# Performance work log

Measured on AMD Instinct MI355X. Metric: run time of the kernel, lower is better.

The kernel has to match this reference:

```python
import jax, jax.numpy as jnp
import numpy as np

N, D, T, E = 50000, 128, 6, 600000
LN_EPS = 1e-5


def setup_inputs() -> dict:
    key = jax.random.key(0)
    ks = jax.random.split(key, 8)
    x = jax.random.normal(ks[0], (N, D), dtype=jnp.float32)
    edge_index = jax.random.randint(ks[1], (2, E), 0, N, dtype=jnp.int64)
    edge_type = jax.random.randint(ks[2], (E,), 0, T, dtype=jnp.int64)
    s = 1.0 / np.sqrt(D)
    W_l = jax.random.normal(ks[3], (T, D, D), dtype=jnp.float32) * s
    W_r = jax.random.normal(ks[4], (T, D, D), dtype=jnp.float32) * s
    b = jax.random.normal(ks[5], (T, D), dtype=jnp.float32) * s
    emb = jax.random.normal(ks[6], (T, D), dtype=jnp.float32)
    gamma = jnp.ones((D,), dtype=jnp.float32)
    beta = jnp.zeros((D,), dtype=jnp.float32)
    return {"x": x, "edge_index": edge_index, "edge_type": edge_type,
            "W_l": W_l, "W_r": W_r, "b": b, "emb": emb,
            "gamma": gamma, "beta": beta}


def reference(x, edge_index, edge_type, W_l, W_r, b, emb, gamma, beta):
    n, d = x.shape
    t = W_l.shape[0]
    src, dst = edge_index[0], edge_index[1]
    # Combined segment id (dst, edge_type) -> one segment_sum for all types.
    seg = dst * t + edge_type
    msgs = x[src]  # (E, d) gathered source features
    sums = jax.ops.segment_sum(msgs, seg, num_segments=n * t).reshape(n, t, d)
    cnt = jax.ops.segment_sum(jnp.ones((seg.shape[0],), x.dtype), seg,
                              num_segments=n * t).reshape(n, t, 1)
    mean = sums / jnp.maximum(cnt, 1.0)  # PyG mean aggr: 0 for isolated nodes
    # Per-type SAGEConv: mean_t @ W_l[t] + x @ W_r[t] + b[t] + emb[t], summed over t.
    h = (jnp.einsum('ntd,tdo->no', mean, W_l)
         + x @ W_r.sum(0)
         + (b.sum(0) + emb.sum(0)))
    mu = jnp.mean(h, axis=-1, keepdims=True)
    var = jnp.var(h, axis=-1, keepdims=True)
    y = (h - mu) * jax.lax.rsqrt(var + LN_EPS) * gamma + beta
    return jax.nn.relu(y)
```

## Files before the change

kernel.cpp:

```cpp
#include <hip/hip_runtime.h>

#define TT 6
#define D 128
#define BM 64
#define CAP 1152
#define SUBCAP 256
#define LN_EPS 1e-5f

typedef __bf16 bf16x8 __attribute__((ext_vector_type(8)));
typedef float f32x4 __attribute__((ext_vector_type(4)));

__device__ __forceinline__ unsigned short f2bf(float f) {
    unsigned int u = __float_as_uint(f);
    unsigned int r = (u + 0x7FFFu + ((u >> 16) & 1u)) >> 16;
    return (unsigned short)r;
}
__device__ __forceinline__ float bflo(unsigned int v) { return __uint_as_float(v << 16); }
__device__ __forceinline__ float bfhi(unsigned int v) { return __uint_as_float(v & 0xffff0000u); }

__device__ __forceinline__ int lds_off128(int row, int kgrp) {
    return row * 128 + (((kgrp & 7) ^ (row & 7)) | (kgrp & 8)) * 8;
}

__global__ void prep_kernel(const float* __restrict__ x, const float* __restrict__ W_l,
                            const float* __restrict__ W_r, const float* __restrict__ b,
                            const float* __restrict__ emb,
                            const int* __restrict__ ei, const int* __restrict__ et,
                            unsigned short* __restrict__ xb, unsigned short* __restrict__ WlT,
                            float* __restrict__ bias_total, int* __restrict__ bcursor,
                            int* __restrict__ ebuf,
                            int total8, int E, int N, int NBK) {
    int i = blockIdx.x * 256 + threadIdx.x;
    if (i < total8) {
        const float4* p = (const float4*)x + (size_t)i * 2;
        float4 a = p[0], bb = p[1];
        uint4 o;
        o.x = (unsigned int)f2bf(a.x) | ((unsigned int)f2bf(a.y) << 16);
        o.y = (unsigned int)f2bf(a.z) | ((unsigned int)f2bf(a.w) << 16);
        o.z = (unsigned int)f2bf(bb.x) | ((unsigned int)f2bf(bb.y) << 16);
        o.w = (unsigned int)f2bf(bb.z) | ((unsigned int)f2bf(bb.w) << 16);
        ((uint4*)xb)[i] = o;
        return;
    }
    i -= total8;
    if (i < 7 * 2048) {
        int s = i >> 11, rem = i & 2047, kg = rem >> 7, n = rem & 127;
        float w[8];
        if (s < TT) {
#pragma unroll
            for (int j = 0; j < 8; ++j)
                w[j] = W_l[s * D * D + (kg * 8 + j) * D + n];
        } else {
#pragma unroll
            for (int j = 0; j < 8; ++j) {
                float sum = 0.f;
#pragma unroll
                for (int t = 0; t < TT; ++t)
                    sum += W_r[t * D * D + (kg * 8 + j) * D + n];
                w[j] = sum;
            }
        }
        uint4 o;
        o.x = (unsigned int)f2bf(w[0]) | ((unsigned int)f2bf(w[1]) << 16);
        o.y = (unsigned int)f2bf(w[2]) | ((unsigned int)f2bf(w[3]) << 16);
        o.z = (unsigned int)f2bf(w[4]) | ((unsigned int)f2bf(w[5]) << 16);
        o.w = (unsigned int)f2bf(w[6]) | ((unsigned int)f2bf(w[7]) << 16);
        *(uint4*)&WlT[(size_t)i * 8] = o;
        return;
    }
    i -= 7 * 2048;
    if (i < D) {
        float s = 0.f;
#pragma unroll
        for (int t = 0; t < TT; ++t) s += b[t * D + i] + emb[t * D + i];
        bias_total[i] = s;
        return;
    }
    i -= D;
    if (i < E) {
        int src = ei[i], dst = ei[E + i], t = et[i];
        int bkt = dst >> 6;
        int shard = blockIdx.x & 7;
        int pos = atomicAdd(&bcursor[(shard * NBK + bkt) * 16], 1);
        if (pos < SUBCAP)
            ebuf[(size_t)bkt * (8 * SUBCAP) + shard * SUBCAP + pos] =
                (src << 9) | ((dst & 63) << 3) | t;
    }
}

__launch_bounds__(256, 3)
__global__ void fused_kernel(const unsigned short* __restrict__ xb,
                             const int* __restrict__ bcursor, const int* __restrict__ ebuf,
                             const unsigned short* __restrict__ WlT,
                             const float* __restrict__ bias_total,
                             const float* __restrict__ gamma, const float* __restrict__ beta,
                             float* __restrict__ out, int N) {
    __shared__ unsigned short As[BM * 128];
    __shared__ int bcnt[TT * BM];
    __shared__ int bcur[TT * BM];
    __shared__ unsigned short esrt[CAP];

    int tid = threadIdx.x;
    int lane = tid & 63, wave = tid >> 6;
    int q = lane >> 4, c16 = lane & 15;
    int qid = tid >> 4, l16 = tid & 15;
    int blockRow = blockIdx.x * BM;
    int NBK = gridDim.x;

    size_t base = (size_t)blockIdx.x * (8 * SUBCAP);
#pragma unroll
    for (int j = 0; j < 2; ++j) {
        int idx = tid + j * 256;
        if (idx < TT * BM) { bcnt[idx] = 0; }
    }
    int pk[8];
#pragma unroll
    for (int j = 0; j < 8; ++j) {
        int bcj = bcursor[(j * NBK + blockIdx.x) * 16];
        if (bcj > SUBCAP) bcj = SUBCAP;
        pk[j] = (tid < bcj) ? ebuf[base + j * SUBCAP + tid] : -1;
    }
    __syncthreads();
#pragma unroll
    for (int j = 0; j < 8; ++j)
        if (pk[j] >= 0) atomicAdd(&bcnt[(pk[j] & 7) * 64 + ((pk[j] >> 3) & 63)], 1);
    __syncthreads();

    if (wave == 0) {
        int c[6];
        int ts = 0;
#pragma unroll
        for (int j = 0; j < 6; ++j) { c[j] = bcnt[lane * 6 + j]; ts += c[j]; }
        int inc = ts;
#pragma unroll
        for (int o = 1; o < 64; o <<= 1) {
            int n = __shfl_up(inc, o);
            if (lane >= o) inc += n;
        }
        int run = inc - ts;
#pragma unroll
        for (int j = 0; j < 6; ++j) { bcur[lane * 6 + j] = run; run += c[j]; }
    }
    __syncthreads();

#pragma unroll
    for (int j = 0; j < 8; ++j)
        if (pk[j] >= 0) {
            int s = (pk[j] & 7) * 64 + ((pk[j] >> 3) & 63);
            int p = atomicAdd(&bcur[s], 1);
            if (p < CAP) esrt[p] = (unsigned short)(pk[j] >> 9);
        }
    __syncthreads();

    f32x4 acc[8];
#pragma unroll
    for (int ct = 0; ct < 8; ++ct) acc[ct] = (f32x4){0.f, 0.f, 0.f, 0.f};

    const unsigned short* Bbase = WlT + ((size_t)q * 128 + c16) * 8;

#pragma unroll 1
    for (int t = 0; t < 7; ++t) {
        bf16x8 afx[4];
        if (t < TT) {
#pragma unroll
            for (int pr = 0; pr < 2; ++pr) {
                int e0[2], cn[2];
#pragma unroll
                for (int i = 0; i < 2; ++i) {
                    int row = qid * 4 + pr * 2 + i;
                    int s = t * 64 + row;
                    int c = bcnt[s];
                    cn[i] = c;
                    e0[i] = bcur[s] - c;
                }
                int ix[2][4];
#pragma unroll
                for (int i = 0; i < 2; ++i)
#pragma unroll
                    for (int j = 0; j < 4; ++j)
                        ix[i][j] = (cn[i] > j) ? (int)esrt[e0[i] + j] : 0;
                uint4 v[2][4];
#pragma unroll
                for (int i = 0; i < 2; ++i)
#pragma unroll
                    for (int j = 0; j < 4; ++j) {
                        v[i][j] = (uint4){0u, 0u, 0u, 0u};
                        if (cn[i] > j)
                            v[i][j] = *(const uint4*)(xb + (size_t)ix[i][j] * D + l16 * 8);
                    }
#pragma unroll
                for (int i = 0; i < 2; ++i) {
                    float a0 = bflo(v[i][0].x) + bflo(v[i][1].x) + bflo(v[i][2].x) + bflo(v[i][3].x);
                    float a1 = bfhi(v[i][0].x) + bfhi(v[i][1].x) + bfhi(v[i][2].x) + bfhi(v[i][3].x);
                    float a2 = bflo(v[i][0].y) + bflo(v[i][1].y) + bflo(v[i][2].y) + bflo(v[i][3].y);
                    float a3 = bfhi(v[i][0].y) + bfhi(v[i][1].y) + bfhi(v[i][2].y) + bfhi(v[i][3].y);
                    float a4 = bflo(v[i][0].z) + bflo(v[i][1].z) + bflo(v[i][2].z) + bflo(v[i][3].z);
                    float a5 = bfhi(v[i][0].z) + bfhi(v[i][1].z) + bfhi(v[i][2].z) + bfhi(v[i][3].z);
                    float a6 = bflo(v[i][0].w) + bflo(v[i][1].w) + bflo(v[i][2].w) + bflo(v[i][3].w);
                    float a7 = bfhi(v[i][0].w) + bfhi(v[i][1].w) + bfhi(v[i][2].w) + bfhi(v[i][3].w);
                    int e = e0[i] + 4, end = e0[i] + cn[i];
#pragma unroll 1
                    while (e < end) {
                        int s = (int)esrt[e++];
                        uint4 vv = *(const uint4*)(xb + (size_t)s * D + l16 * 8);
                        a0 += bflo(vv.x); a1 += bfhi(vv.x);
                        a2 += bflo(vv.y); a3 += bfhi(vv.y);
                        a4 += bflo(vv.z); a5 += bfhi(vv.z);
                        a6 += bflo(vv.w); a7 += bfhi(vv.w);
                    }
                    if (cn[i] > 1) {
                        float sc = 1.f / (float)cn[i];
                        a0 *= sc; a1 *= sc; a2 *= sc; a3 *= sc;
                        a4 *= sc; a5 *= sc; a6 *= sc; a7 *= sc;
                    }
                    uint4 p;
                    p.x = (unsigned int)f2bf(a0) | ((unsigned int)f2bf(a1) << 16);
                    p.y = (unsigned int)f2bf(a2) | ((unsigned int)f2bf(a3) << 16);
                    p.z = (unsigned int)f2bf(a4) | ((unsigned int)f2bf(a5) << 16);
                    p.w = (unsigned int)f2bf(a6) | ((unsigned int)f2bf(a7) << 16);
                    *(uint4*)&As[lds_off128(qid * 4 + pr * 2 + i, l16)] = p;
                }
            }
        } else {
            int gr = blockRow + wave * 16 + c16; if (gr >= N) gr = N - 1;
#pragma unroll
            for (int ks = 0; ks < 4; ++ks)
                afx[ks] = *(const bf16x8*)(xb + (size_t)gr * D + (ks * 4 + q) * 8);
        }

        const unsigned short* Bt = Bbase + (size_t)t * 16384;
#pragma unroll
        for (int ks = 0; ks < 4; ++ks) {
            bf16x8 af;
            if (t < TT)
                af = *(const bf16x8*)&As[lds_off128(wave * 16 + c16, ks * 4 + q)];
            else
                af = afx[ks];
#pragma unroll
            for (int ct = 0; ct < 8; ++ct) {
                bf16x8 bfr = *(const bf16x8*)(Bt + ks * 4096 + ct * 128);
                acc[ct] = __builtin_amdgcn_mfma_f32_16x16x32_bf16(af, bfr, acc[ct], 0, 0, 0);
            }
        }
    }

    float bias_c[8], g_c[8], bt_c[8];
#pragma unroll
    for (int ct = 0; ct < 8; ++ct) {
        int col = ct * 16 + c16;
        bias_c[ct] = bias_total[col];
        g_c[ct] = gamma[col];
        bt_c[ct] = beta[col];
    }
#pragma unroll
    for (int reg = 0; reg < 4; ++reg) {
        float h[8];
        float s = 0.f, s2 = 0.f;
#pragma unroll
        for (int ct = 0; ct < 8; ++ct) {
            h[ct] = acc[ct][reg] + bias_c[ct];
            s += h[ct];
            s2 += h[ct] * h[ct];
        }
#pragma unroll
        for (int o = 8; o >= 1; o >>= 1) {
            s  += __shfl_xor(s, o, 16);
            s2 += __shfl_xor(s2, o, 16);
        }
        float mu = s * (1.f / 128.f);
        float var = s2 * (1.f / 128.f) - mu * mu;
        float rstd = rsqrtf(var + LN_EPS);
        int row = blockRow + wave * 16 + q * 4 + reg;
        if (row < N) {
#pragma unroll
            for (int ct = 0; ct < 8; ++ct) {
                float y = (h[ct] - mu) * rstd * g_c[ct] + bt_c[ct];
                out[(size_t)row * D + ct * 16 + c16] = fmaxf(y, 0.f);
            }
        }
    }
}

extern "C" void kernel_launch(void* const* d_in, const int* in_sizes, int n_in,
                              void* d_out, int out_size, void* d_ws, size_t ws_size,
                              hipStream_t stream) {
    const float* x     = (const float*)d_in[0];
    const int*   ei    = (const int*)d_in[1];
    const int*   et    = (const int*)d_in[2];
    const float* W_l   = (const float*)d_in[3];
    const float* W_r   = (const float*)d_in[4];
    const float* b     = (const float*)d_in[5];
    const float* emb   = (const float*)d_in[6];
    const float* gamma = (const float*)d_in[7];
    const float* beta  = (const float*)d_in[8];

    int N = in_sizes[0] / D;
    int E = in_sizes[2];
    int NBLK = (N + BM - 1) / BM;

    int* bcursor = (int*)d_ws;
    int* ebuf    = bcursor + 8 * NBLK * 16;
    size_t ofs = (size_t)((char*)(ebuf + (size_t)NBLK * 8 * SUBCAP) - (char*)d_ws);
    ofs = (ofs + 15) & ~(size_t)15;
    unsigned short* WlT = (unsigned short*)((char*)d_ws + ofs);
    float* bias_total = (float*)(WlT + 7 * 2048 * 8);
    size_t ofs2 = (size_t)((char*)(bias_total + D) - (char*)d_ws);
    ofs2 = (ofs2 + 15) & ~(size_t)15;
    unsigned short* xb = (unsigned short*)((char*)d_ws + ofs2);

    hipMemsetAsync(bcursor, 0, (size_t)(8 * NBLK * 16) * sizeof(int), stream);

    int total8 = N * D / 8;
    int G = total8 + 7 * 2048 + D + E;
    prep_kernel<<<(G + 255) / 256, 256, 0, stream>>>(x, W_l, W_r, b, emb, ei, et,
                                                     xb, WlT, bias_total, bcursor, ebuf,
                                                     total8, E, N, NBLK);

    fused_kernel<<<NBLK, 256, 0, stream>>>(xb, bcursor, ebuf, WlT, bias_total,
                                           gamma, beta, (float*)d_out, N);
}
```

Before: 182.2 us.

## Merge prep and fused kernels into one persistent kernel with grid barrier

Folds the preprocessing work (bf16 conversion of x and weights, bias sum, edge bucketing) into the main kernel as a grid-stride loop. A software global barrier on an atomic counter separates it from the aggregation/GEMM/LayerNorm phase. This removes one kernel launch and the gap between launches. The barrier relies on all 782 blocks being co-resident; at 3 blocks/CU on 256 CUs that holds, but otherwise it would deadlock. The shard index now depends on a different block mapping, which changes sub-bucket contention.

```diff
diff --git a/kernel.cpp b/kernel.cpp
--- a/kernel.cpp
+++ b/kernel.cpp
@@ -22,92 +22,96 @@
     return row * 128 + (((kgrp & 7) ^ (row & 7)) | (kgrp & 8)) * 8;
 }
 
-__global__ void prep_kernel(const float* __restrict__ x, const float* __restrict__ W_l,
+__launch_bounds__(256, 3)
+__global__ void mega_kernel(const float* __restrict__ x, const float* __restrict__ W_l,
                             const float* __restrict__ W_r, const float* __restrict__ b,
                             const float* __restrict__ emb,
                             const int* __restrict__ ei, const int* __restrict__ et,
                             unsigned short* __restrict__ xb, unsigned short* __restrict__ WlT,
                             float* __restrict__ bias_total, int* __restrict__ bcursor,
-                            int* __restrict__ ebuf,
-                            int total8, int E, int N, int NBK) {
-    int i = blockIdx.x * 256 + threadIdx.x;
-    if (i < total8) {
-        const float4* p = (const float4*)x + (size_t)i * 2;
-        float4 a = p[0], bb = p[1];
-        uint4 o;
-        o.x = (unsigned int)f2bf(a.x) | ((unsigned int)f2bf(a.y) << 16);
-        o.y = (unsigned int)f2bf(a.z) | ((unsigned int)f2bf(a.w) << 16);
-        o.z = (unsigned int)f2bf(bb.x) | ((unsigned int)f2bf(bb.y) << 16);
-        o.w = (unsigned int)f2bf(bb.z) | ((unsigned int)f2bf(bb.w) << 16);
-        ((uint4*)xb)[i] = o;
-        return;
-    }
-    i -= total8;
-    if (i < 7 * 2048) {
-        int s = i >> 11, rem = i & 2047, kg = rem >> 7, n = rem & 127;
-        float w[8];
-        if (s < TT) {
-#pragma unroll
-            for (int j = 0; j < 8; ++j)
-                w[j] = W_l[s * D * D + (kg * 8 + j) * D + n];
-        } else {
-#pragma unroll
-            for (int j = 0; j < 8; ++j) {
-                float sum = 0.f;
-#pragma unroll
-                for (int t = 0; t < TT; ++t)
-                    sum += W_r[t * D * D + (kg * 8 + j) * D + n];
-                w[j] = sum;
-            }
-        }
-        uint4 o;
-        o.x = (unsigned int)f2bf(w[0]) | ((unsigned int)f2bf(w[1]) << 16);
-        o.y = (unsigned int)f2bf(w[2]) | ((unsigned int)f2bf(w[3]) << 16);
-        o.z = (unsigned int)f2bf(w[4]) | ((unsigned int)f2bf(w[5]) << 16);
-        o.w = (unsigned int)f2bf(w[6]) | ((unsigned int)f2bf(w[7]) << 16);
-        *(uint4*)&WlT[(size_t)i * 8] = o;
-        return;
-    }
-    i -= 7 * 2048;
-    if (i < D) {
-        float s = 0.f;
-#pragma unroll
-        for (int t = 0; t < TT; ++t) s += b[t * D + i] + emb[t * D + i];
-        bias_total[i] = s;
-        return;
-    }
-    i -= D;
-    if (i < E) {
-        int src = ei[i], dst = ei[E + i], t = et[i];
-        int bkt = dst >> 6;
-        int shard = blockIdx.x & 7;
-        int pos = atomicAdd(&bcursor[(shard * NBK + bkt) * 16], 1);
-        if (pos < SUBCAP)
-            ebuf[(size_t)bkt * (8 * SUBCAP) + shard * SUBCAP + pos] =
-                (src << 9) | ((dst & 63) << 3) | t;
-    }
-}
-
-__launch_bounds__(256, 3)
-__global__ void fused_kernel(const unsigned short* __restrict__ xb,
-                             const int* __restrict__ bcursor, const int* __restrict__ ebuf,
-                             const unsigned short* __restrict__ WlT,
-                             const float* __restrict__ bias_total,
-                             const float* __restrict__ gamma, const float* __restrict__ beta,
-                             float* __restrict__ out, int N) {
+                            int* __restrict__ gctr, int* __restrict__ ebuf,
+                            const float* __restrict__ gamma, const float* __restrict__ beta,
+                            float* __restrict__ out,
+                            int total8, int E, int N) {
     __shared__ unsigned short As[BM * 128];
     __shared__ int bcnt[TT * BM];
     __shared__ int bcur[TT * BM];
     __shared__ unsigned short esrt[CAP];
 
     int tid = threadIdx.x;
+    int bid = blockIdx.x;
+    int NBK = gridDim.x;
+
+    int G = total8 + 7 * 2048 + D + E;
+    int stride = NBK * 256;
+    for (int i = bid * 256 + tid; i < G; i += stride) {
+        int j = i;
+        if (j < total8) {
+            const float4* p = (const float4*)x + (size_t)j * 2;
+            float4 a = p[0], bb = p[1];
+            uint4 o;
+            o.x = (unsigned int)f2bf(a.x) | ((unsigned int)f2bf(a.y) << 16);
+            o.y = (unsigned int)f2bf(a.z) | ((unsigned int)f2bf(a.w) << 16);
+            o.z = (unsigned int)f2bf(bb.x) | ((unsigned int)f2bf(bb.y) << 16);
+            o.w = (unsigned int)f2bf(bb.z) | ((unsigned int)f2bf(bb.w) << 16);
+            ((uint4*)xb)[j] = o;
+        } else if ((j -= total8) < 7 * 2048) {
+            int s = j >> 11, rem = j & 2047, kg = rem >> 7, n = rem & 127;
+            float w[8];
+            if (s < TT) {
+#pragma unroll
+                for (int k = 0; k < 8; ++k)
+                    w[k] = W_l[s * D * D + (kg * 8 + k) * D + n];
+            } else {
+#pragma unroll
+                for (int k = 0; k < 8; ++k) {
+                    float sum = 0.f;
+#pragma unroll
+                    for (int t = 0; t < TT; ++t)
+                        sum += W_r[t * D * D + (kg * 8 + k) * D + n];
+                    w[k] = sum;
+                }
+            }
+            uint4 o;
+            o.x = (unsigned int)f2bf(w[0]) | ((unsigned int)f2bf(w[1]) << 16);
+            o.y = (unsigned int)f2bf(w[2]) | ((unsigned int)f2bf(w[3]) << 16);
+            o.z = (unsigned int)f2bf(w[4]) | ((unsigned int)f2bf(w[5]) << 16);
+            o.w = (unsigned int)f2bf(w[6]) | ((unsigned int)f2bf(w[7]) << 16);
+            *(uint4*)&WlT[(size_t)j * 8] = o;
+        } else if ((j -= 7 * 2048) < D) {
+            float s = 0.f;
+#pragma unroll
+            for (int t = 0; t < TT; ++t) s += b[t * D + j] + emb[t * D + j];
+            bias_total[j] = s;
+        } else {
+            j -= D;
+            int src = ei[j], dst = ei[E + j], t = et[j];
+            int bkt = dst >> 6;
+            int shard = bid & 7;
+            int pos = atomicAdd(&bcursor[(shard * NBK + bkt) * 16], 1);
+            if (pos < SUBCAP)
+                ebuf[(size_t)bkt * (8 * SUBCAP) + shard * SUBCAP + pos] =
+                    (src << 9) | ((dst & 63) << 3) | t;
+        }
+    }
+
+    __syncthreads();
+    if (tid == 0) {
+        __threadfence();
+        atomicAdd(gctr, 1);
+        while (atomicAdd(gctr, 0) < (int)gridDim.x) {
+            __builtin_amdgcn_s_sleep(2);
+        }
+        __threadfence();
+    }
+    __syncthreads();
+
     int lane = tid & 63, wave = tid >> 6;
     int q = lane >> 4, c16 = lane & 15;
     int qid = tid >> 4, l16 = tid & 15;
-    int blockRow = blockIdx.x * BM;
-    int NBK = gridDim.x;
-
-    size_t base = (size_t)blockIdx.x * (8 * SUBCAP);
+    int blockRow = bid * BM;
+
+    size_t base = (size_t)bid * (8 * SUBCAP);
 #pragma unroll
     for (int j = 0; j < 2; ++j) {
         int idx = tid + j * 256;
@@ -116,7 +120,7 @@
     int pk[8];
 #pragma unroll
     for (int j = 0; j < 8; ++j) {
-        int bcj = bcursor[(j * NBK + blockIdx.x) * 16];
+        int bcj = bcursor[(j * NBK + bid) * 16];
         if (bcj > SUBCAP) bcj = SUBCAP;
         pk[j] = (tid < bcj) ? ebuf[base + j * SUBCAP + tid] : -1;
     }
@@ -299,7 +303,8 @@
     int NBLK = (N + BM - 1) / BM;
 
     int* bcursor = (int*)d_ws;
-    int* ebuf    = bcursor + 8 * NBLK * 16;
+    int* gctr    = bcursor + 8 * NBLK * 16;
+    int* ebuf    = gctr + 16;
     size_t ofs = (size_t)((char*)(ebuf + (size_t)NBLK * 8 * SUBCAP) - (char*)d_ws);
     ofs = (ofs + 15) & ~(size_t)15;
     unsigned short* WlT = (unsigned short*)((char*)d_ws + ofs);
@@ -308,14 +313,11 @@
     ofs2 = (ofs2 + 15) & ~(size_t)15;
     unsigned short* xb = (unsigned short*)((char*)d_ws + ofs2);
 
-    hipMemsetAsync(bcursor, 0, (size_t)(8 * NBLK * 16) * sizeof(int), stream);
+    hipMemsetAsync(bcursor, 0, (size_t)(8 * NBLK * 16 + 16) * sizeof(int), stream);
 
     int total8 = N * D / 8;
-    int G = total8 + 7 * 2048 + D + E;
-    prep_kernel<<<(G + 255) / 256, 256, 0, stream>>>(x, W_l, W_r, b, emb, ei, et,
-                                                     xb, WlT, bias_total, bcursor, ebuf,
-                                                     total8, E, N, NBLK);
-
-    fused_kernel<<<NBLK, 256, 0, stream>>>(xb, bcursor, ebuf, WlT, bias_total,
-                                           gamma, beta, (float*)d_out, N);
+    mega_kernel<<<NBLK, 256, 0, stream>>>(x, W_l, W_r, b, emb, ei, et,
+                                          xb, WlT, bias_total, bcursor, gctr, ebuf,
+                                          gamma, beta, (float*)d_out,
+                                          total8, E, N);
 }
```

Result: slower. 278.4 us (+52.8%).
